# Performance work log

Measured on AMD Instinct MI355X. Metric: run time of the kernel, lower is better.

## Reference

```python
import jax, jax.numpy as jnp
import numpy as np


def _rgcn(x, src, dst, et, basis, comp, root, bias):
    # Basis-decomposed RGCNConv (PyG semantics): per-relation mean aggregation
    # over incoming edges + root transform + bias.
    N = x.shape[0]
    R = comp.shape[0]
    W = jnp.einsum('rb,bio->rio', comp, basis)          # [R, in, out]
    xr = jnp.einsum('ni,rio->rno', x, W)                 # [R, N, out]
    msg = xr[et, src]                                    # [E, out] gather per edge
    seg = dst * R + et                                   # (target, relation) segment id
    cnt = jax.ops.segment_sum(jnp.ones(et.shape, x.dtype), seg, num_segments=N * R)
    norm = 1.0 / jnp.maximum(cnt, 1.0)                   # mean per (dst, relation)
    msg = msg * norm[seg][:, None]
    agg = jax.ops.segment_sum(msg, dst, num_segments=N)  # scatter-add to targets
    return agg + x @ root + bias


def setup_inputs() -> dict:
    key = jax.random.key(0)
    ks = jax.random.split(key, 20)
    N, E, R, B, F, D, C, NB = 100000, 1600000, 5, 512, 4, 32, 5, 2
    s = 0.1
    inp = {
        'x': jax.random.normal(ks[0], (N, F), jnp.float32),
        'edge_index': jax.random.randint(ks[1], (2, E), 0, N, dtype=jnp.int32),
        'edge_type': jax.random.randint(ks[2], (E,), 0, R, dtype=jnp.int32),
        'start_nodes': jax.random.randint(ks[3], (B,), 0, N, dtype=jnp.int32),
        # layer 0: in=F, out=D
        'basis0': jax.random.normal(ks[4], (NB, F, D), jnp.float32) * s,
        'comp0': jax.random.normal(ks[5], (R, NB), jnp.float32) * s,
        'root0': jax.random.normal(ks[6], (F, D), jnp.float32) * s,
        'bias0': jax.random.normal(ks[7], (D,), jnp.float32) * s,
        # layers 1..3: in=out=D, stacked
        'basis': jax.random.normal(ks[8], (3, NB, D, D), jnp.float32) * s,
        'comp': jax.random.normal(ks[9], (3, R, NB), jnp.float32) * s,
        'root': jax.random.normal(ks[10], (3, D, D), jnp.float32) * s,
        'bias': jax.random.normal(ks[11], (3, D), jnp.float32) * s,
        # MLP head: sum(latent_dim)=128 -> 128 -> C
        'lin1_w': jax.random.normal(ks[12], (4 * D, 128), jnp.float32) * s,
        'lin1_b': jax.random.normal(ks[13], (128,), jnp.float32) * s,
        'lin2_w': jax.random.normal(ks[14], (128, C), jnp.float32) * s,
        'lin2_b': jax.random.normal(ks[15], (C,), jnp.float32) * s,
    }
    return inp


def reference(x, edge_index, edge_type, start_nodes, basis0, comp0, root0, bias0,
              basis, comp, root, bias, lin1_w, lin1_b, lin2_w, lin2_b):
    src, dst = edge_index[0], edge_index[1]
    h = jnp.tanh(_rgcn(x, src, dst, edge_type, basis0, comp0, root0, bias0))
    states = [h]
    for l in range(basis.shape[0]):
        h = jnp.tanh(_rgcn(h, src, dst, edge_type, basis[l], comp[l], root[l], bias[l]))
        states.append(h)
    concat = jnp.concatenate(states, axis=1)             # [N, 128]
    # Per-graph readout: the walk's degenerate n_walks=1 branch, i.e. the
    # start (user) node's concatenated state (sequential backtracking walk
    # replaced by its deterministic initialization path; eval mode, no dropout).
    acc = concat[start_nodes]                            # [B, 128]
    h1 = jax.nn.relu(acc @ lin1_w + lin1_b)
    logits = h1 @ lin2_w + lin2_b
    return jax.nn.log_softmax(logits, axis=-1)
```

## Files before the change

### kernel.cpp

```cpp
#include <hip/hip_runtime.h>
#include <cstdint>

#define N_NODES 100000
#define N_EDGES 1600000
#define R_REL   5
#define NBASIS  2
#define B_START 512
#define NBUCK   256
#define BUCK_SZ 391
#define EPB     6250
#define STAGE_CAP 7000

__device__ __forceinline__ unsigned short f2bf(float f) {
    unsigned u = __float_as_uint(f);
    unsigned r = (u + 0x7FFF + ((u >> 16) & 1)) >> 16;
    return (unsigned short)r;
}


__global__ __launch_bounds__(256) void k_cntb(
    const int* __restrict__ ei, int* __restrict__ bhist) {
    __shared__ int lh[NBUCK];
    int tid = threadIdx.x;
    lh[tid] = 0;
    __syncthreads();
    int base = blockIdx.x * EPB;
    for (int j = tid; j < EPB; j += 256) {
        int dst = ei[N_EDGES + base + j];
        atomicAdd(&lh[dst / BUCK_SZ], 1);
    }
    __syncthreads();
    bhist[blockIdx.x * NBUCK + tid] = lh[tid];
}

__global__ __launch_bounds__(256) void k_scanb(
    int* __restrict__ bhist, int* __restrict__ bbase) {
    int b = threadIdx.x;
    int tot = 0;
    for (int i = 0; i < NBUCK; i += 8) {
        int v0 = bhist[(i + 0) * NBUCK + b], v1 = bhist[(i + 1) * NBUCK + b];
        int v2 = bhist[(i + 2) * NBUCK + b], v3 = bhist[(i + 3) * NBUCK + b];
        int v4 = bhist[(i + 4) * NBUCK + b], v5 = bhist[(i + 5) * NBUCK + b];
        int v6 = bhist[(i + 6) * NBUCK + b], v7 = bhist[(i + 7) * NBUCK + b];
        tot += v0 + v1 + v2 + v3 + v4 + v5 + v6 + v7;
    }
    __shared__ int s[NBUCK];
    s[b] = tot;
    __syncthreads();
    for (int o = 1; o < NBUCK; o <<= 1) {
        int v = (b >= o) ? s[b - o] : 0;
        __syncthreads();
        s[b] += v;
        __syncthreads();
    }
    int base = s[b] - tot;
    bbase[b] = base;
    if (b == NBUCK - 1) bbase[NBUCK] = s[NBUCK - 1];
    int run = base;
    for (int i = 0; i < NBUCK; i += 8) {
        int v0 = bhist[(i + 0) * NBUCK + b], v1 = bhist[(i + 1) * NBUCK + b];
        int v2 = bhist[(i + 2) * NBUCK + b], v3 = bhist[(i + 3) * NBUCK + b];
        int v4 = bhist[(i + 4) * NBUCK + b], v5 = bhist[(i + 5) * NBUCK + b];
        int v6 = bhist[(i + 6) * NBUCK + b], v7 = bhist[(i + 7) * NBUCK + b];
        bhist[(i + 0) * NBUCK + b] = run; run += v0;
        bhist[(i + 1) * NBUCK + b] = run; run += v1;
        bhist[(i + 2) * NBUCK + b] = run; run += v2;
        bhist[(i + 3) * NBUCK + b] = run; run += v3;
        bhist[(i + 4) * NBUCK + b] = run; run += v4;
        bhist[(i + 5) * NBUCK + b] = run; run += v5;
        bhist[(i + 6) * NBUCK + b] = run; run += v6;
        bhist[(i + 7) * NBUCK + b] = run; run += v7;
    }
}

__global__ __launch_bounds__(256) void k_scat(
    const int* __restrict__ ei, const int* __restrict__ et,
    const int* __restrict__ bhist, int* __restrict__ arena) {
    __shared__ int lc[NBUCK];
    int tid = threadIdx.x;
    lc[tid] = bhist[blockIdx.x * NBUCK + tid];
    __syncthreads();
    int base = blockIdx.x * EPB;
    for (int j = tid; j < EPB; j += 256) {
        int e   = base + j;
        int src = ei[e];
        int dst = ei[N_EDGES + e];
        int t   = et[e];
        int bk  = dst / BUCK_SZ;
        int dl  = dst - bk * BUCK_SZ;
        int pos = atomicAdd(&lc[bk], 1);
        arena[pos] = src | (t << 17) | (dl << 20);
    }
}

__global__ __launch_bounds__(256) void k_build(
    const int* __restrict__ arena, const int* __restrict__ bbase,
    int* __restrict__ pk_m, float* __restrict__ pk_nv,
    int* __restrict__ pk_dst) {
    __shared__ int deg5[BUCK_SZ * R_REL];
    __shared__ int loff[BUCK_SZ + 1];
    __shared__ int cur[BUCK_SZ];
    __shared__ int stg[STAGE_CAP];
    int b = blockIdx.x, tid = threadIdx.x;
    int base = bbase[b], end = bbase[b + 1];
    int count = end - base;
    for (int i = tid; i < BUCK_SZ * R_REL; i += 256) deg5[i] = 0;
    __syncthreads();
    for (int i = tid; i < count; i += 256) {
        int r  = arena[base + i];
        int dl = ((unsigned)r) >> 20;
        int t  = (r >> 17) & 7;
        atomicAdd(&deg5[dl * R_REL + t], 1);
    }
    __syncthreads();
    if (tid == 0) {
        int run = 0;
        for (int dl = 0; dl < BUCK_SZ; dl++) {
            loff[dl] = run;
            run += deg5[dl * R_REL + 0] + deg5[dl * R_REL + 1] +
                   deg5[dl * R_REL + 2] + deg5[dl * R_REL + 3] +
                   deg5[dl * R_REL + 4];
        }
        loff[BUCK_SZ] = run;
    }
    __syncthreads();
    for (int dl = tid; dl < BUCK_SZ; dl += 256) cur[dl] = loff[dl];
    __syncthreads();
    for (int i = tid; i < count; i += 256) {
        int r  = arena[base + i];
        int dl = ((unsigned)r) >> 20;
        int rk = atomicAdd(&cur[dl], 1);
        if (rk < STAGE_CAP) stg[rk] = r;
    }
    __syncthreads();
    for (int i = tid; i < count; i += 256) {
        int r   = stg[i < STAGE_CAP ? i : STAGE_CAP - 1];
        int src = r & 0x1FFFF;
        int t   = (r >> 17) & 7;
        int dl  = ((unsigned)r) >> 20;
        int c   = deg5[dl * R_REL + t];
        pk_m[base + i]   = src | (t << 17);
        pk_nv[base + i]  = 1.0f / (float)(c > 0 ? c : 1);
        pk_dst[base + i] = b * BUCK_SZ + dl;
    }
}


template <int IN, bool TIN>
__global__ __launch_bounds__(256) void k_xform(
    const float* __restrict__ h_in, float* __restrict__ h_out,
    unsigned short* __restrict__ y5, const float* __restrict__ basis,
    const float* __restrict__ root, const float* __restrict__ biasL,
    const float* __restrict__ compL, const int* __restrict__ start,
    float* __restrict__ sav) {
    int tid  = threadIdx.x;
    int lane = tid & 31;
    int sub  = tid >> 5;
    int g    = blockIdx.x * 8 + sub;
    if (IN == 32 && sav != nullptr && g < B_START) {
        int row = start[g];
        sav[g * 32 + lane] = tanhf(h_in[row * 32 + lane]);
    }
    float w0[IN], w1[IN], wr[IN];
#pragma unroll
    for (int i = 0; i < IN; i++) {
        w0[i] = basis[i * 32 + lane];
        w1[i] = basis[IN * 32 + i * 32 + lane];
        wr[i] = root[i * 32 + lane];
    }
    float c0[R_REL], c1[R_REL];
#pragma unroll
    for (int r = 0; r < R_REL; r++) {
        c0[r] = compL[r * NBASIS + 0];
        c1[r] = compL[r * NBASIS + 1];
    }
    float bv = biasL[lane];
    for (int n = g; n < N_NODES; n += 8192) {
        float hn = (lane < IN) ? h_in[n * IN + lane] : 0.f;
        if (TIN) hn = tanhf(hn);
        float a0 = 0.f, a1 = 0.f, ar = bv;
#pragma unroll
        for (int i = 0; i < IN; i++) {
            float v = __shfl(hn, i, 32);
            a0 += v * w0[i];
            a1 += v * w1[i];
            ar += v * wr[i];
        }
#pragma unroll
        for (int r = 0; r < R_REL; r++)
            y5[(size_t)r * N_NODES * 32 + n * 32 + lane] = f2bf(c0[r] * a0 + c1[r] * a1);
        h_out[n * 32 + lane] = ar;
    }
}


__global__ __launch_bounds__(256) void k_edge(
    const unsigned short* __restrict__ y5, float* __restrict__ h,
    const int* __restrict__ pk_m, const float* __restrict__ pk_nv,
    const int* __restrict__ pk_dst) {
    int tid  = threadIdx.x;
    int lane = tid & 31;
    int sub  = tid >> 5;
    int run  = blockIdx.x * 8 + sub;
    int base = run * 32;
    if (base >= N_EDGES) return;
    int idx = base + lane;
    int   m  = pk_m[idx];
    float nv = pk_nv[idx];
    int   d  = pk_dst[idx];

    float acc = 0.f;
    int dcur = __shfl(d, 0, 32);
#pragma unroll
    for (int j = 0; j < 32; j += 8) {
        int mm[8];
#pragma unroll
        for (int q = 0; q < 8; q++) mm[q] = __shfl(m, j + q, 32);
        unsigned short uu[8];
#pragma unroll
        for (int q = 0; q < 8; q++) {
            unsigned r = ((unsigned)mm[q] >> 17) * N_NODES + (mm[q] & 0x1FFFF);
            uu[q] = y5[(size_t)r * 32 + lane];
        }
        float val[8];
#pragma unroll
        for (int q = 0; q < 8; q++)
            val[q] = __shfl(nv, j + q, 32) *
                     __uint_as_float((unsigned)uu[q] << 16);
#pragma unroll
        for (int q = 0; q < 8; q++) {
            int dj = __shfl(d, j + q, 32);
            if (dj != dcur) {
                atomicAdd(&h[(size_t)dcur * 32 + lane], acc);
                acc = 0.f;
                dcur = dj;
            }
            acc += val[q];
        }
    }
    atomicAdd(&h[(size_t)dcur * 32 + lane], acc);
}


__global__ void k_saveT(const float* __restrict__ h, const int* __restrict__ start,
                        float* __restrict__ sav) {
    int t = blockIdx.x * blockDim.x + threadIdx.x;
    if (t < B_START * 32) {
        int b = t >> 5, ln = t & 31;
        sav[t] = tanhf(h[start[b] * 32 + ln]);
    }
}

__global__ __launch_bounds__(128) void k_mlp(
    const float* __restrict__ sav, const float* __restrict__ w1,
    const float* __restrict__ b1, const float* __restrict__ w2,
    const float* __restrict__ b2, float* __restrict__ out) {
    __shared__ float cvec[128];
    __shared__ float hb[128];
    __shared__ float lg[8];
    int b = blockIdx.x, t = threadIdx.x;
    cvec[t] = sav[(t >> 5) * (B_START * 32) + b * 32 + (t & 31)];
    __syncthreads();
    float a = b1[t];
#pragma unroll 8
    for (int k = 0; k < 128; k++) a += cvec[k] * w1[k * 128 + t];
    hb[t] = fmaxf(a, 0.f);
    __syncthreads();
    if (t < 5) {
        float a2 = b2[t];
        for (int k = 0; k < 128; k++) a2 += hb[k] * w2[k * 5 + t];
        lg[t] = a2;
    }
    __syncthreads();
    if (t < 5) {
        float m = lg[0];
        for (int j = 1; j < 5; j++) m = fmaxf(m, lg[j]);
        float s = 0.f;
        for (int j = 0; j < 5; j++) s += expf(lg[j] - m);
        out[b * 5 + t] = lg[t] - m - logf(s);
    }
}


extern "C" void kernel_launch(void* const* d_in, const int* in_sizes, int n_in,
                              void* d_out, int out_size, void* d_ws, size_t ws_size,
                              hipStream_t stream) {
    const float* x      = (const float*)d_in[0];
    const int*   ei     = (const int*)d_in[1];
    const int*   etype  = (const int*)d_in[2];
    const int*   start  = (const int*)d_in[3];
    const float* basis0 = (const float*)d_in[4];
    const float* comp0  = (const float*)d_in[5];
    const float* root0  = (const float*)d_in[6];
    const float* bias0  = (const float*)d_in[7];
    const float* basis  = (const float*)d_in[8];
    const float* comp   = (const float*)d_in[9];
    const float* root   = (const float*)d_in[10];
    const float* bias   = (const float*)d_in[11];
    const float* w1     = (const float*)d_in[12];
    const float* b1     = (const float*)d_in[13];
    const float* w2     = (const float*)d_in[14];
    const float* b2     = (const float*)d_in[15];
    float* out = (float*)d_out;

    char* p = (char*)d_ws;
    auto alloc = [&](size_t bytes) -> void* {
        void* r = (void*)p;
        p += (bytes + 255) & ~(size_t)255;
        return r;
    };
    int*            bhist  = (int*)alloc((size_t)NBUCK * NBUCK * 4);
    int*            bbase  = (int*)alloc((NBUCK + 1) * 4);
    int*            arena  = (int*)alloc((size_t)N_EDGES * 4);
    int*            pk_m   = (int*)alloc((size_t)N_EDGES * 4);
    float*          pk_nv  = (float*)alloc((size_t)N_EDGES * 4);
    int*            pk_dst = (int*)alloc((size_t)N_EDGES * 4);
    float*          hA     = (float*)alloc((size_t)N_NODES * 32 * 4);
    float*          hB     = (float*)alloc((size_t)N_NODES * 32 * 4);
    unsigned short* y5     = (unsigned short*)alloc((size_t)R_REL * N_NODES * 32 * 2);
    float*          sav    = (float*)alloc(4 * B_START * 32 * 4);

    k_cntb<<<NBUCK, 256, 0, stream>>>(ei, bhist);
    k_scanb<<<1, 256, 0, stream>>>(bhist, bbase);
    k_scat<<<NBUCK, 256, 0, stream>>>(ei, etype, bhist, arena);
    k_build<<<NBUCK, 256, 0, stream>>>(arena, bbase, pk_m, pk_nv, pk_dst);

    int nbEdge = (N_EDGES / 32 + 7) / 8;
    k_xform<4, false><<<1024, 256, 0, stream>>>(x, hA, y5, basis0, root0,
                                                bias0, comp0, start, nullptr);
    k_edge<<<nbEdge, 256, 0, stream>>>(y5, hA, pk_m, pk_nv, pk_dst);
    float* hin = hA;
    float* hout = hB;
    for (int l = 0; l < 3; l++) {
        k_xform<32, true><<<1024, 256, 0, stream>>>(
            hin, hout, y5, basis + (size_t)l * 2048, root + (size_t)l * 1024,
            bias + l * 32, comp + l * 10, start, sav + l * 16384);
        k_edge<<<nbEdge, 256, 0, stream>>>(y5, hout, pk_m, pk_nv, pk_dst);
        float* tmp = hin; hin = hout; hout = tmp;
    }
    k_saveT<<<64, 256, 0, stream>>>(hin, start, sav + 3 * 16384);

    k_mlp<<<B_START, 128, 0, stream>>>(sav, w1, b1, w2, b2, out);
}
```

Baseline: 411.5 us.

## Stage gathered bf16 rows into LDS with 16-byte vector loads in edge kernel

The edge aggregation kernel now has each 64-lane wave gather its 64 edge source rows with int4 loads, four lanes per 64-byte row, into shared memory. Each half-wave then reduces 32 edges from LDS using segmented accumulation and atomics as before. This replaces scattered 2-byte per-lane global loads with wide vector loads to cut memory transactions. The cost is added LDS traffic and a block-wide barrier, and the grid size changes to exactly E/256 with no bounds check.

```diff
diff --git a/kernel.cpp b/kernel.cpp
--- a/kernel.cpp
+++ b/kernel.cpp
@@ -198,47 +198,44 @@
     const unsigned short* __restrict__ y5, float* __restrict__ h,
     const int* __restrict__ pk_m, const float* __restrict__ pk_nv,
     const int* __restrict__ pk_dst) {
-    int tid  = threadIdx.x;
-    int lane = tid & 31;
-    int sub  = tid >> 5;
-    int run  = blockIdx.x * 8 + sub;
-    int base = run * 32;
-    if (base >= N_EDGES) return;
-    int idx = base + lane;
-    int   m  = pk_m[idx];
-    float nv = pk_nv[idx];
-    int   d  = pk_dst[idx];
-
+    __shared__ unsigned short rows[4][64][32];
+    int tid = threadIdx.x;
+    int wv  = tid >> 6;
+    int ln  = tid & 63;
+    int ebase = (blockIdx.x * 4 + wv) * 64;
+    int e = ebase + ln;
+    int   mL  = pk_m[e];
+    float nvL = pk_nv[e];
+    int   dL  = pk_dst[e];
+
+    int team = ln >> 2, tl = ln & 3;
+    const int4* __restrict__ y4 = (const int4*)y5;
+#pragma unroll
+    for (int r = 0; r < 4; r++) {
+        int m = __shfl(mL, r * 16 + team, 64);
+        unsigned row = ((unsigned)m >> 17) * N_NODES + (m & 0x1FFFF);
+        int4 v = y4[(size_t)row * 4 + tl];
+        ((int4*)&rows[wv][r * 16 + team][0])[tl] = v;
+    }
+    __syncthreads();
+
+    int c = ln & 31;
+    const unsigned short* myrows = &rows[wv][(ln >> 5) * 32][0];
     float acc = 0.f;
-    int dcur = __shfl(d, 0, 32);
-#pragma unroll
-    for (int j = 0; j < 32; j += 8) {
-        int mm[8];
-#pragma unroll
-        for (int q = 0; q < 8; q++) mm[q] = __shfl(m, j + q, 32);
-        unsigned short uu[8];
-#pragma unroll
-        for (int q = 0; q < 8; q++) {
-            unsigned r = ((unsigned)mm[q] >> 17) * N_NODES + (mm[q] & 0x1FFFF);
-            uu[q] = y5[(size_t)r * 32 + lane];
+    int dcur = __shfl(dL, 0, 32);
+#pragma unroll
+    for (int j = 0; j < 32; j++) {
+        float nv = __shfl(nvL, j, 32);
+        int   dj = __shfl(dL, j, 32);
+        float val = nv * __uint_as_float((unsigned)myrows[j * 32 + c] << 16);
+        if (dj != dcur) {
+            atomicAdd(&h[(size_t)dcur * 32 + c], acc);
+            acc = 0.f;
+            dcur = dj;
         }
-        float val[8];
-#pragma unroll
-        for (int q = 0; q < 8; q++)
-            val[q] = __shfl(nv, j + q, 32) *
-                     __uint_as_float((unsigned)uu[q] << 16);
-#pragma unroll
-        for (int q = 0; q < 8; q++) {
-            int dj = __shfl(d, j + q, 32);
-            if (dj != dcur) {
-                atomicAdd(&h[(size_t)dcur * 32 + lane], acc);
-                acc = 0.f;
-                dcur = dj;
-            }
-            acc += val[q];
-        }
-    }
-    atomicAdd(&h[(size_t)dcur * 32 + lane], acc);
+        acc += val;
+    }
+    atomicAdd(&h[(size_t)dcur * 32 + c], acc);
 }
 
 
@@ -325,7 +322,7 @@
     k_scat<<<NBUCK, 256, 0, stream>>>(ei, etype, bhist, arena);
     k_build<<<NBUCK, 256, 0, stream>>>(arena, bbase, pk_m, pk_nv, pk_dst);
 
-    int nbEdge = (N_EDGES / 32 + 7) / 8;
+    int nbEdge = N_EDGES / 256;
     k_xform<4, false><<<1024, 256, 0, stream>>>(x, hA, y5, basis0, root0,
                                                 bias0, comp0, start, nullptr);
     k_edge<<<nbEdge, 256, 0, stream>>>(y5, hA, pk_m, pk_nv, pk_dst);
```

Result: no change. 414.5 us (+0.7%).
